# Kernel tuning notes

Measured on AMD Instinct MI355X. Metric: run time of the kernel, lower is better.

Reference implementation:

```python
import jax, jax.numpy as jnp
import numpy as np

B = 16        # number of lists
N = 1024      # items per list (all equal)
D = 256       # feature dim (= dim_emb, need_embedding=False)


def setup_inputs() -> dict:
    key = jax.random.key(0)
    k1, k2, k3 = jax.random.split(key, 3)
    feats = jax.random.normal(k1, (B * N, D), dtype=jnp.float32)
    length = jnp.full((B,), N, dtype=jnp.int32)
    # Bilinear params: torch nn.Bilinear(d, d, 1) -> weight [1, d, d], bias [1]
    # xavier_uniform on the 3-d weight: bound = sqrt(6 / (fan_in + fan_out)) with
    # fan_in = d (last dim), fan_out = 1*d (per torch _calculate_fan_in_and_fan_out)
    bound = float(np.sqrt(6.0 / (D + D)))
    W_upper = jax.random.uniform(k2, (1, D, D), jnp.float32, -bound, bound)
    W_lower = jax.random.uniform(k3, (1, D, D), jnp.float32, -bound, bound)
    b_upper = jnp.zeros((1,), jnp.float32)
    b_lower = jnp.zeros((1,), jnp.float32)
    return {"feats": feats, "W_upper": W_upper, "b_upper": b_upper,
            "W_lower": W_lower, "b_lower": b_lower, "length": length}


def reference(feats, W_upper, b_upper, W_lower, b_lower, length):
    # nb_layers=0, need_embedding=False -> embedding and transformer are Identity.
    b = length.shape[0]
    n = feats.shape[0] // b  # equal-length lists -> static reshape
    d = feats.shape[-1]
    X = feats.reshape(b, n, d)  # [B, n, d]
    # For list i: repeated_feats_1 row (p*n + q) = x_p, repeated_feats_2 row = x_q,
    # so adjacency[p, q] = x_p^T W x_q + bias  (Bilinear with out=1).
    upper = jnp.einsum('bnd,de,bme->bnm', X, W_upper[0], X) + b_upper[0]
    lower = jnp.einsum('bnd,de,bme->bnm', X, W_lower[0], X) + b_lower[0]
    adj = jnp.triu(upper) + jnp.tril(lower, -1)  # [B, n, n]
    return adj
```

## Files before the change

kernel.cpp:

```cpp
#include <hip/hip_runtime.h>

#define BL 16
#define NL 1024
#define DD 256

typedef short bf16x8 __attribute__((ext_vector_type(8)));
typedef float f32x4 __attribute__((ext_vector_type(4)));

static __device__ __forceinline__ short f32_to_bf16(float f) {
  union { float f; unsigned u; } v; v.f = f;
  unsigned r = (v.u + 0x7FFFu + ((v.u >> 16) & 1u)) >> 16;
  return (short)r;
}

static __device__ __forceinline__ void g2l16(const short* g, short* l) {
  __builtin_amdgcn_global_load_lds(
      (const __attribute__((address_space(1))) void*)g,
      (__attribute__((address_space(3))) void*)l, 16, 0, 0);
}

static __device__ __forceinline__ void stage_tile(const short* __restrict__ gbase,
                                                  short* __restrict__ lds,
                                                  int t, int k0) {
  const int row = t >> 2, kc = t & 3;
#pragma unroll
  for (int i = 0; i < 2; ++i) {
    const short* g = gbase + (size_t)(row + 64 * i) * DD + k0 + kc * 8;
    g2l16(g, lds + i * 2048 + t * 8);
  }
}

static __device__ __forceinline__ void mma_step(const short* __restrict__ As,
                                                const short* __restrict__ Bs,
                                                int wm, int wn, int r, int quad,
                                                f32x4 acc[4][4]) {
  bf16x8 af[4], bf[4];
#pragma unroll
  for (int i = 0; i < 4; ++i) {
    af[i] = *(const bf16x8*)(As + (wm + i * 16 + r) * 32 + quad * 8);
    bf[i] = *(const bf16x8*)(Bs + (wn + i * 16 + r) * 32 + quad * 8);
  }
#pragma unroll
  for (int mt = 0; mt < 4; ++mt)
#pragma unroll
    for (int nt = 0; nt < 4; ++nt)
      acc[mt][nt] = __builtin_amdgcn_mfma_f32_16x16x32_bf16(af[mt], bf[nt], acc[mt][nt], 0, 0, 0);
}

__global__ __launch_bounds__(256) void k_prep(const float* __restrict__ X,
                                              const float* __restrict__ Wu,
                                              const float* __restrict__ Wl,
                                              short* __restrict__ Xb,
                                              short* __restrict__ WTu,
                                              short* __restrict__ WTl) {
  const int bid = blockIdx.x;
  if (bid < 4096) {
    int i = bid * 256 + threadIdx.x;
    const float4 v = ((const float4*)X)[i];
    short4 o;
    o.x = f32_to_bf16(v.x); o.y = f32_to_bf16(v.y);
    o.z = f32_to_bf16(v.z); o.w = f32_to_bf16(v.w);
    ((short4*)Xb)[i] = o;
  } else {
    const int id = bid - 4096;
    const int z = id >> 8, d = id & 255;
    const float* W = z ? Wl : Wu;
    short* WT = z ? WTl : WTu;
    const int e = threadIdx.x;
    WT[e * DD + d] = f32_to_bf16(W[d * DD + e]);
  }
}

__global__ __launch_bounds__(256) void k_stage1(const short* __restrict__ Xb,
                                                const short* __restrict__ WTu,
                                                const short* __restrict__ WTl,
                                                short* __restrict__ YU,
                                                short* __restrict__ YL) {
  __shared__ short As[2][128 * 32], Bs[2][128 * 32];
  const short* Bt = blockIdx.z ? WTl : WTu;
  short* Y = blockIdx.z ? YL : YU;
  const int m0 = blockIdx.y * 128, n0 = blockIdx.x * 128;
  const int t = threadIdx.x, lane = t & 63, wave = t >> 6;
  const int r = lane & 15, quad = lane >> 4;
  const int wm = (wave >> 1) * 64, wn = (wave & 1) * 64;
  f32x4 acc[4][4] = {};
  const short* Ag = Xb + (size_t)m0 * DD;
  const short* Bg = Bt + (size_t)n0 * DD;
  for (int k0 = 0; k0 < DD; k0 += 64) {
    stage_tile(Ag, As[0], t, k0);
    stage_tile(Ag, As[1], t, k0 + 32);
    stage_tile(Bg, Bs[0], t, k0);
    stage_tile(Bg, Bs[1], t, k0 + 32);
    __syncthreads();
    mma_step(As[0], Bs[0], wm, wn, r, quad, acc);
    mma_step(As[1], Bs[1], wm, wn, r, quad, acc);
    __syncthreads();
  }
#pragma unroll
  for (int mt = 0; mt < 4; ++mt)
#pragma unroll
    for (int nt = 0; nt < 4; ++nt)
#pragma unroll
      for (int i = 0; i < 4; ++i)
        Y[(size_t)(m0 + wm + mt * 16 + quad * 4 + i) * DD + n0 + wn + nt * 16 + r] =
            f32_to_bf16(acc[mt][nt][i]);
}

__global__ __launch_bounds__(256) void k_stage2_off(const short* __restrict__ Xb,
                                                    const short* __restrict__ YU,
                                                    const short* __restrict__ YL,
                                                    const float* __restrict__ bu_p,
                                                    const float* __restrict__ bl_p,
                                                    float* __restrict__ out) {
  __shared__ short As[2][128 * 32], Bs[2][128 * 32];
  const int idx = blockIdx.x, b = blockIdx.y;
  const int pt = idx / 7, j = idx % 7;
  const int qt = j + (j >= pt ? 1 : 0);
  const size_t off = (size_t)b * NL * DD;
  const short* Ag = ((qt > pt) ? YU : YL) + off + (size_t)pt * 128 * DD;
  const short* Bg = Xb + off + (size_t)qt * 128 * DD;
  const float bias = (qt > pt) ? bu_p[0] : bl_p[0];
  const int t = threadIdx.x, lane = t & 63, wave = t >> 6;
  const int r = lane & 15, quad = lane >> 4;
  const int wm = (wave >> 1) * 64, wn = (wave & 1) * 64;
  const f32x4 binit = {bias, bias, bias, bias};
  f32x4 acc[4][4];
#pragma unroll
  for (int mt = 0; mt < 4; ++mt)
#pragma unroll
    for (int nt = 0; nt < 4; ++nt) acc[mt][nt] = binit;
  for (int k0 = 0; k0 < DD; k0 += 64) {
    stage_tile(Ag, As[0], t, k0);
    stage_tile(Ag, As[1], t, k0 + 32);
    stage_tile(Bg, Bs[0], t, k0);
    stage_tile(Bg, Bs[1], t, k0 + 32);
    __syncthreads();
    mma_step(As[0], Bs[0], wm, wn, r, quad, acc);
    mma_step(As[1], Bs[1], wm, wn, r, quad, acc);
    __syncthreads();
  }
  float* Ob = out + (size_t)b * NL * NL;
  const int p0 = pt * 128 + wm, q0 = qt * 128 + wn;
#pragma unroll
  for (int mt = 0; mt < 4; ++mt)
#pragma unroll
    for (int nt = 0; nt < 4; ++nt)
#pragma unroll
      for (int i = 0; i < 4; ++i)
        Ob[(size_t)(p0 + mt * 16 + quad * 4 + i) * NL + q0 + nt * 16 + r] =
            acc[mt][nt][i];
}

__global__ __launch_bounds__(256) void k_stage2_diag(const short* __restrict__ Xb,
                                                     const short* __restrict__ YU,
                                                     const short* __restrict__ YL,
                                                     const float* __restrict__ bu_p,
                                                     const float* __restrict__ bl_p,
                                                     float* __restrict__ out) {
  __shared__ short Au[2][128 * 32], Al[2][128 * 32], Bs[2][128 * 32];
  const int pt = blockIdx.x, b = blockIdx.y;
  const size_t off = (size_t)b * NL * DD;
  const short* Agu = YU + off + (size_t)pt * 128 * DD;
  const short* Agl = YL + off + (size_t)pt * 128 * DD;
  const short* Bg = Xb + off + (size_t)pt * 128 * DD;
  const float bu = bu_p[0], bl = bl_p[0];
  const int t = threadIdx.x, lane = t & 63, wave = t >> 6;
  const int r = lane & 15, quad = lane >> 4;
  const int wm = (wave >> 1) * 64, wn = (wave & 1) * 64;
  f32x4 accU[4][4] = {}, accL[4][4] = {};
  for (int k0 = 0; k0 < DD; k0 += 64) {
    stage_tile(Agu, Au[0], t, k0);
    stage_tile(Agu, Au[1], t, k0 + 32);
    stage_tile(Agl, Al[0], t, k0);
    stage_tile(Agl, Al[1], t, k0 + 32);
    stage_tile(Bg, Bs[0], t, k0);
    stage_tile(Bg, Bs[1], t, k0 + 32);
    __syncthreads();
    mma_step(Au[0], Bs[0], wm, wn, r, quad, accU);
    mma_step(Al[0], Bs[0], wm, wn, r, quad, accL);
    mma_step(Au[1], Bs[1], wm, wn, r, quad, accU);
    mma_step(Al[1], Bs[1], wm, wn, r, quad, accL);
    __syncthreads();
  }
  float* Ob = out + (size_t)b * NL * NL;
  const int p0 = pt * 128 + wm, q0 = pt * 128 + wn;
#pragma unroll
  for (int mt = 0; mt < 4; ++mt)
#pragma unroll
    for (int nt = 0; nt < 4; ++nt)
#pragma unroll
      for (int i = 0; i < 4; ++i) {
        const int p = p0 + mt * 16 + quad * 4 + i;
        const int q = q0 + nt * 16 + r;
        Ob[(size_t)p * NL + q] =
            (q >= p) ? (accU[mt][nt][i] + bu) : (accL[mt][nt][i] + bl);
      }
}

extern "C" void kernel_launch(void* const* d_in, const int* in_sizes, int n_in,
                              void* d_out, int out_size, void* d_ws, size_t ws_size,
                              hipStream_t stream) {
  const float* feats = (const float*)d_in[0];
  const float* Wu    = (const float*)d_in[1];
  const float* bu    = (const float*)d_in[2];
  const float* Wl    = (const float*)d_in[3];
  const float* bl    = (const float*)d_in[4];
  float* out = (float*)d_out;

  char* ws = (char*)d_ws;
  short* Xb  = (short*)(ws);
  short* YU  = (short*)(ws + (size_t)8 * 1024 * 1024);
  short* YL  = (short*)(ws + (size_t)16 * 1024 * 1024);
  short* WTu = (short*)(ws + (size_t)24 * 1024 * 1024);
  short* WTl = (short*)(ws + (size_t)24 * 1024 * 1024 + DD * DD * 2);

  k_prep<<<4096 + 512, 256, 0, stream>>>(feats, Wu, Wl, Xb, WTu, WTl);

  k_stage1<<<dim3(DD / 128, BL * NL / 128, 2), 256, 0, stream>>>(Xb, WTu, WTl, YU, YL);

  k_stage2_off<<<dim3(56, BL), 256, 0, stream>>>(Xb, YU, YL, bu, bl, out);
  k_stage2_diag<<<dim3(8, BL), 256, 0, stream>>>(Xb, YU, YL, bu, bl, out);
}
```

Measured before the change: 134.4 us.

## Swizzle bf16 global layout, double-buffer K loop, merge stage2 kernels

Stores Xb, WT and Y in an XOR-swizzled chunk layout so the direct global-to-LDS copies land in bank-conflict-free positions for the MFMA fragment reads. The K loop becomes a 32-wide double-buffered pipeline that prefetches the next tile while computing the current one, with a single barrier per step. The off-diagonal and diagonal stage2 kernels are merged into one launch in which diagonal tiles run two passes, removing a kernel launch. Diagonal blocks now cost twice as long as the others, which creates some load imbalance.

```diff
diff --git a/kernel.cpp b/kernel.cpp
--- a/kernel.cpp
+++ b/kernel.cpp
@@ -3,6 +3,7 @@
 #define BL 16
 #define NL 1024
 #define DD 256
+#define KSTEPS 8
 
 typedef short bf16x8 __attribute__((ext_vector_type(8)));
 typedef float f32x4 __attribute__((ext_vector_type(4)));
@@ -19,6 +20,7 @@
       (__attribute__((address_space(3))) void*)l, 16, 0, 0);
 }
 
+
 static __device__ __forceinline__ void stage_tile(const short* __restrict__ gbase,
                                                   short* __restrict__ lds,
                                                   int t, int k0) {
@@ -34,17 +36,24 @@
                                                 const short* __restrict__ Bs,
                                                 int wm, int wn, int r, int quad,
                                                 f32x4 acc[4][4]) {
+  const int ch = (quad ^ ((r >> 1) & 3)) * 8;
   bf16x8 af[4], bf[4];
 #pragma unroll
   for (int i = 0; i < 4; ++i) {
-    af[i] = *(const bf16x8*)(As + (wm + i * 16 + r) * 32 + quad * 8);
-    bf[i] = *(const bf16x8*)(Bs + (wn + i * 16 + r) * 32 + quad * 8);
+    af[i] = *(const bf16x8*)(As + (wm + i * 16 + r) * 32 + ch);
+    bf[i] = *(const bf16x8*)(Bs + (wn + i * 16 + r) * 32 + ch);
   }
 #pragma unroll
   for (int mt = 0; mt < 4; ++mt)
 #pragma unroll
     for (int nt = 0; nt < 4; ++nt)
       acc[mt][nt] = __builtin_amdgcn_mfma_f32_16x16x32_bf16(af[mt], bf[nt], acc[mt][nt], 0, 0, 0);
+}
+
+static __device__ __forceinline__ size_t sw_off(int row, int k) {
+  const int panel = k >> 5, c = (k >> 3) & 3, j = k & 7;
+  const int s = (row >> 1) & 3;
+  return (size_t)row * DD + panel * 32 + ((c ^ s) * 8) + j;
 }
 
 __global__ __launch_bounds__(256) void k_prep(const float* __restrict__ X,
@@ -54,20 +63,23 @@
                                               short* __restrict__ WTu,
                                               short* __restrict__ WTl) {
   const int bid = blockIdx.x;
-  if (bid < 4096) {
-    int i = bid * 256 + threadIdx.x;
-    const float4 v = ((const float4*)X)[i];
-    short4 o;
-    o.x = f32_to_bf16(v.x); o.y = f32_to_bf16(v.y);
-    o.z = f32_to_bf16(v.z); o.w = f32_to_bf16(v.w);
-    ((short4*)Xb)[i] = o;
+  if (bid < 2048) {
+    const int i = bid * 256 + threadIdx.x;
+    const int row = i >> 5, c32 = i & 31;
+    const int panel = c32 >> 2, c = c32 & 3;
+    const float4* src = (const float4*)(X + (size_t)row * DD + panel * 32 + c * 8);
+    const float4 v0 = src[0], v1 = src[1];
+    short o[8] = {f32_to_bf16(v0.x), f32_to_bf16(v0.y), f32_to_bf16(v0.z), f32_to_bf16(v0.w),
+                  f32_to_bf16(v1.x), f32_to_bf16(v1.y), f32_to_bf16(v1.z), f32_to_bf16(v1.w)};
+    const int s = (row >> 1) & 3;
+    *(bf16x8*)(Xb + (size_t)row * DD + panel * 32 + ((c ^ s) * 8)) = *(bf16x8*)o;
   } else {
-    const int id = bid - 4096;
+    const int id = bid - 2048;
     const int z = id >> 8, d = id & 255;
     const float* W = z ? Wl : Wu;
     short* WT = z ? WTl : WTu;
     const int e = threadIdx.x;
-    WT[e * DD + d] = f32_to_bf16(W[d * DD + e]);
+    WT[sw_off(e, d)] = f32_to_bf16(W[d * DD + e]);
   }
 }
 
@@ -86,15 +98,15 @@
   f32x4 acc[4][4] = {};
   const short* Ag = Xb + (size_t)m0 * DD;
   const short* Bg = Bt + (size_t)n0 * DD;
-  for (int k0 = 0; k0 < DD; k0 += 64) {
-    stage_tile(Ag, As[0], t, k0);
-    stage_tile(Ag, As[1], t, k0 + 32);
-    stage_tile(Bg, Bs[0], t, k0);
-    stage_tile(Bg, Bs[1], t, k0 + 32);
+  stage_tile(Ag, As[0], t, 0);
+  stage_tile(Bg, Bs[0], t, 0);
+  for (int i = 0; i < KSTEPS; ++i) {
     __syncthreads();
-    mma_step(As[0], Bs[0], wm, wn, r, quad, acc);
-    mma_step(As[1], Bs[1], wm, wn, r, quad, acc);
-    __syncthreads();
+    if (i + 1 < KSTEPS) {
+      stage_tile(Ag, As[(i + 1) & 1], t, (i + 1) * 32);
+      stage_tile(Bg, Bs[(i + 1) & 1], t, (i + 1) * 32);
+    }
+    mma_step(As[i & 1], Bs[i & 1], wm, wn, r, quad, acc);
   }
 #pragma unroll
   for (int mt = 0; mt < 4; ++mt)
@@ -102,99 +114,63 @@
     for (int nt = 0; nt < 4; ++nt)
 #pragma unroll
       for (int i = 0; i < 4; ++i)
-        Y[(size_t)(m0 + wm + mt * 16 + quad * 4 + i) * DD + n0 + wn + nt * 16 + r] =
+        Y[sw_off(m0 + wm + mt * 16 + quad * 4 + i, n0 + wn + nt * 16 + r)] =
             f32_to_bf16(acc[mt][nt][i]);
 }
 
-__global__ __launch_bounds__(256) void k_stage2_off(const short* __restrict__ Xb,
-                                                    const short* __restrict__ YU,
-                                                    const short* __restrict__ YL,
-                                                    const float* __restrict__ bu_p,
-                                                    const float* __restrict__ bl_p,
-                                                    float* __restrict__ out) {
+__global__ __launch_bounds__(256) void k_stage2(const short* __restrict__ Xb,
+                                                const short* __restrict__ YU,
+                                                const short* __restrict__ YL,
+                                                const float* __restrict__ bu_p,
+                                                const float* __restrict__ bl_p,
+                                                float* __restrict__ out) {
   __shared__ short As[2][128 * 32], Bs[2][128 * 32];
-  const int idx = blockIdx.x, b = blockIdx.y;
-  const int pt = idx / 7, j = idx % 7;
-  const int qt = j + (j >= pt ? 1 : 0);
+  const int pt = blockIdx.x >> 3, qt = blockIdx.x & 7, b = blockIdx.y;
   const size_t off = (size_t)b * NL * DD;
-  const short* Ag = ((qt > pt) ? YU : YL) + off + (size_t)pt * 128 * DD;
   const short* Bg = Xb + off + (size_t)qt * 128 * DD;
-  const float bias = (qt > pt) ? bu_p[0] : bl_p[0];
   const int t = threadIdx.x, lane = t & 63, wave = t >> 6;
   const int r = lane & 15, quad = lane >> 4;
   const int wm = (wave >> 1) * 64, wn = (wave & 1) * 64;
-  const f32x4 binit = {bias, bias, bias, bias};
-  f32x4 acc[4][4];
-#pragma unroll
-  for (int mt = 0; mt < 4; ++mt)
-#pragma unroll
-    for (int nt = 0; nt < 4; ++nt) acc[mt][nt] = binit;
-  for (int k0 = 0; k0 < DD; k0 += 64) {
-    stage_tile(Ag, As[0], t, k0);
-    stage_tile(Ag, As[1], t, k0 + 32);
-    stage_tile(Bg, Bs[0], t, k0);
-    stage_tile(Bg, Bs[1], t, k0 + 32);
-    __syncthreads();
-    mma_step(As[0], Bs[0], wm, wn, r, quad, acc);
-    mma_step(As[1], Bs[1], wm, wn, r, quad, acc);
-    __syncthreads();
-  }
   float* Ob = out + (size_t)b * NL * NL;
   const int p0 = pt * 128 + wm, q0 = qt * 128 + wn;
+  const float bu = bu_p[0], bl = bl_p[0];
+  const bool diag = (pt == qt);
+  const int npass = diag ? 2 : 1;
+
+  for (int pass = 0; pass < npass; ++pass) {
+    const bool useU = diag ? (pass == 0) : (qt > pt);
+    const short* Ag = (useU ? YU : YL) + off + (size_t)pt * 128 * DD;
+    const float bias = useU ? bu : bl;
+    const f32x4 binit = {bias, bias, bias, bias};
+    f32x4 acc[4][4];
 #pragma unroll
-  for (int mt = 0; mt < 4; ++mt)
+    for (int mt = 0; mt < 4; ++mt)
 #pragma unroll
-    for (int nt = 0; nt < 4; ++nt)
+      for (int nt = 0; nt < 4; ++nt) acc[mt][nt] = binit;
+
+    __syncthreads();
+    stage_tile(Ag, As[0], t, 0);
+    stage_tile(Bg, Bs[0], t, 0);
+    for (int i = 0; i < KSTEPS; ++i) {
+      __syncthreads();
+      if (i + 1 < KSTEPS) {
+        stage_tile(Ag, As[(i + 1) & 1], t, (i + 1) * 32);
+        stage_tile(Bg, Bs[(i + 1) & 1], t, (i + 1) * 32);
+      }
+      mma_step(As[i & 1], Bs[i & 1], wm, wn, r, quad, acc);
+    }
 #pragma unroll
-      for (int i = 0; i < 4; ++i)
-        Ob[(size_t)(p0 + mt * 16 + quad * 4 + i) * NL + q0 + nt * 16 + r] =
-            acc[mt][nt][i];
-}
-
-__global__ __launch_bounds__(256) void k_stage2_diag(const short* __restrict__ Xb,
-                                                     const short* __restrict__ YU,
-                                                     const short* __restrict__ YL,
-                                                     const float* __restrict__ bu_p,
-                                                     const float* __restrict__ bl_p,
-                                                     float* __restrict__ out) {
-  __shared__ short Au[2][128 * 32], Al[2][128 * 32], Bs[2][128 * 32];
-  const int pt = blockIdx.x, b = blockIdx.y;
-  const size_t off = (size_t)b * NL * DD;
-  const short* Agu = YU + off + (size_t)pt * 128 * DD;
-  const short* Agl = YL + off + (size_t)pt * 128 * DD;
-  const short* Bg = Xb + off + (size_t)pt * 128 * DD;
-  const float bu = bu_p[0], bl = bl_p[0];
-  const int t = threadIdx.x, lane = t & 63, wave = t >> 6;
-  const int r = lane & 15, quad = lane >> 4;
-  const int wm = (wave >> 1) * 64, wn = (wave & 1) * 64;
-  f32x4 accU[4][4] = {}, accL[4][4] = {};
-  for (int k0 = 0; k0 < DD; k0 += 64) {
-    stage_tile(Agu, Au[0], t, k0);
-    stage_tile(Agu, Au[1], t, k0 + 32);
-    stage_tile(Agl, Al[0], t, k0);
-    stage_tile(Agl, Al[1], t, k0 + 32);
-    stage_tile(Bg, Bs[0], t, k0);
-    stage_tile(Bg, Bs[1], t, k0 + 32);
-    __syncthreads();
-    mma_step(Au[0], Bs[0], wm, wn, r, quad, accU);
-    mma_step(Al[0], Bs[0], wm, wn, r, quad, accL);
-    mma_step(Au[1], Bs[1], wm, wn, r, quad, accU);
-    mma_step(Al[1], Bs[1], wm, wn, r, quad, accL);
-    __syncthreads();
+    for (int mt = 0; mt < 4; ++mt)
+#pragma unroll
+      for (int nt = 0; nt < 4; ++nt)
+#pragma unroll
+        for (int i = 0; i < 4; ++i) {
+          const int p = p0 + mt * 16 + quad * 4 + i;
+          const int q = q0 + nt * 16 + r;
+          if (!diag || (pass == 0 ? (q >= p) : (q < p)))
+            Ob[(size_t)p * NL + q] = acc[mt][nt][i];
+        }
   }
-  float* Ob = out + (size_t)b * NL * NL;
-  const int p0 = pt * 128 + wm, q0 = pt * 128 + wn;
-#pragma unroll
-  for (int mt = 0; mt < 4; ++mt)
-#pragma unroll
-    for (int nt = 0; nt < 4; ++nt)
-#pragma unroll
-      for (int i = 0; i < 4; ++i) {
-        const int p = p0 + mt * 16 + quad * 4 + i;
-        const int q = q0 + nt * 16 + r;
-        Ob[(size_t)p * NL + q] =
-            (q >= p) ? (accU[mt][nt][i] + bu) : (accL[mt][nt][i] + bl);
-      }
 }
 
 extern "C" void kernel_launch(void* const* d_in, const int* in_sizes, int n_in,
@@ -214,10 +190,9 @@
   short* WTu = (short*)(ws + (size_t)24 * 1024 * 1024);
   short* WTl = (short*)(ws + (size_t)24 * 1024 * 1024 + DD * DD * 2);
 
-  k_prep<<<4096 + 512, 256, 0, stream>>>(feats, Wu, Wl, Xb, WTu, WTl);
+  k_prep<<<2048 + 512, 256, 0, stream>>>(feats, Wu, Wl, Xb, WTu, WTl);
 
   k_stage1<<<dim3(DD / 128, BL * NL / 128, 2), 256, 0, stream>>>(Xb, WTu, WTl, YU, YL);
 
-  k_stage2_off<<<dim3(56, BL), 256, 0, stream>>>(Xb, YU, YL, bu, bl, out);
-  k_stage2_diag<<<dim3(8, BL), 256, 0, stream>>>(Xb, YU, YL, bu, bl, out);
+  k_stage2<<<dim3(64, BL), 256, 0, stream>>>(Xb, YU, YL, bu, bl, out);
 }
```

Result: slower. 139.0 us (+3.4%).
